# Optimization experiments

Measured on AMD Instinct MI355X. Metric: run time of the kernel, lower is better.

## Reference

```python
import jax, jax.numpy as jnp
import numpy as np
import math

_DENSE_LOCAL_W = 64
_DYADIC = [96, 128, 192, 256, 384, 512, 768, 1024, 1536]
OFFSETS = sorted(set(range(0, _DENSE_LOCAL_W + 1)) | set(_DYADIC))  # 74 offsets

B, N, D, H = 1, 2048, 1024, 16
HD = D // H


def setup_inputs() -> dict:
    key = jax.random.key(0)
    ks = jax.random.split(key, 8)
    s = 1.0 / math.sqrt(D)
    x = jax.random.normal(ks[0], (B, N, D), dtype=jnp.float32)
    Wqkv = jax.random.uniform(ks[1], (3 * D, D), jnp.float32, -s, s)
    bqkv = jax.random.uniform(ks[2], (3 * D,), jnp.float32, -s, s)
    Wgate = jax.random.uniform(ks[3], (D, D), jnp.float32, -s, s)
    bgate = jax.random.uniform(ks[4], (D,), jnp.float32, -s, s)
    Wout = jax.random.uniform(ks[5], (D, D), jnp.float32, -s, s)
    bout = jax.random.uniform(ks[6], (D,), jnp.float32, -s, s)
    # pos_bias init exactly as in the module: -log(1+delta) * alpha_h, shape (O, H)
    alphas = jnp.linspace(0.2, 2.0, H)
    deltas = jnp.array([math.log(1.0 + d) for d in OFFSETS], dtype=jnp.float32)
    pos_bias = -deltas[:, None] * alphas[None, :]
    offsets = jnp.array(OFFSETS, dtype=jnp.int32)
    return {"x": x, "Wqkv": Wqkv, "bqkv": bqkv, "Wgate": Wgate, "bgate": bgate,
            "Wout": Wout, "bout": bout, "pos_bias": pos_bias, "offsets": offsets}


def reference(x, Wqkv, bqkv, Wgate, bgate, Wout, bout, pos_bias, offsets):
    Bx, Nx, Dx = x.shape
    qkv = x @ Wqkv.T + bqkv                       # (B, N, 3D)
    q, k, v = jnp.split(qkv, 3, axis=-1)
    q = q.reshape(Bx, Nx, H, HD).transpose(0, 2, 1, 3)  # (B, H, N, HD)
    k = k.reshape(Bx, Nx, H, HD).transpose(0, 2, 1, 3)
    v = v.reshape(Bx, Nx, H, HD).transpose(0, 2, 1, 3)
    scale = HD ** -0.5

    # gather shifted K/V: position n attends to n - delta for each fixed offset
    n_idx = jnp.arange(Nx, dtype=jnp.int32)[:, None]      # (N, 1)
    idx = n_idx - offsets[None, :]                        # (N, O)
    valid = idx >= 0                                      # (N, O)
    idx_c = jnp.clip(idx, 0, Nx - 1)
    K_all = k[:, :, idx_c, :]                             # (B, H, N, O, HD)
    V_all = v[:, :, idx_c, :]

    scores = jnp.einsum('bhnd,bhnod->bhno', q, K_all) * scale
    scores = scores + pos_bias.T[None, :, None, :]        # (1, H, 1, O)
    scores = jnp.where(valid[None, None], scores, -jnp.inf)
    alpha = jax.nn.softmax(scores, axis=-1)               # (B, H, N, O)
    out = jnp.einsum('bhno,bhnod->bhnd', alpha, V_all)    # (B, H, N, HD)

    flat = out.transpose(0, 2, 1, 3).reshape(Bx, Nx, Dx)  # (B, N, D)
    gate = jax.nn.sigmoid(x @ Wgate.T + bgate)
    return (flat * gate) @ Wout.T + bout                  # dropout = identity (eval)
```

## Files before the change

### kernel.cpp

```cpp
#include <hip/hip_runtime.h>
#include <hip/hip_bf16.h>

#define SEQ_N 2048
#define DIM   1024
#define NHEAD 16
#define HDIM  64
#define LDQ   4096
#define NOFF  74
#define NDENSE 65
#define NJ    224
#define NT    16
#define PST   232
#define QST   88

typedef __attribute__((ext_vector_type(8))) __bf16 bv8;
typedef __attribute__((ext_vector_type(4))) __bf16 bv4;
typedef __attribute__((ext_vector_type(4))) float  f32x4;

typedef __attribute__((address_space(3))) void as3_void;
typedef __attribute__((address_space(1))) void as1_void;

__device__ __forceinline__ void async16(const void* g, void* l) {
  __builtin_amdgcn_global_load_lds((as1_void*)(unsigned long long)g,
                                   (as3_void*)l, 16, 0, 0);
}

#define E1 (SEQ_N * DIM)
#define E2 (E1 + 3 * DIM * DIM)
#define E3 (E2 + DIM * DIM)
#define E4 (E3 + DIM * DIM)
__global__ __launch_bounds__(256) void cvt_all(
    const float* __restrict__ x, const float* __restrict__ wqkv,
    const float* __restrict__ wgate, const float* __restrict__ wout,
    __bf16* __restrict__ dst) {
  long i = ((long)blockIdx.x * 256 + threadIdx.x) * 4;
  if (i >= E4) return;
  const float* s; long o;
  if (i < E1)      { s = x;     o = i; }
  else if (i < E2) { s = wqkv;  o = i - E1; }
  else if (i < E3) { s = wgate; o = i - E2; }
  else             { s = wout;  o = i - E3; }
  float4 v = *(const float4*)(s + o);
  bv4 ov;
  ov[0] = (__bf16)v.x; ov[1] = (__bf16)v.y; ov[2] = (__bf16)v.z; ov[3] = (__bf16)v.w;
  *(bv4*)(dst + i) = ov;
}

#define BM 128
#define BK 32

template <int BN_, typename OutT>
__global__ __launch_bounds__(256) void gemm_bt(
    const __bf16* __restrict__ A, const __bf16* __restrict__ B1,
    const __bf16* __restrict__ B2, const float* __restrict__ bias1,
    const float* __restrict__ bias2, int Nsplit,
    OutT* __restrict__ C, int ldc, int K) {
  __shared__ __attribute__((aligned(16))) __bf16 Asm[BM * BK];
  __shared__ __attribute__((aligned(16))) __bf16 Bsm[BN_ * BK];
  constexpr int NJT = BN_ / 32;
  constexpr int CA = BM * BK / 8;
  constexpr int CB = BN_ * BK / 8;

  const int tid  = threadIdx.x;
  const int lane = tid & 63;
  const int wave = tid >> 6;
  const int wr = wave >> 1, wc = wave & 1;
  const int fr = lane & 15, fq = lane >> 4;

  const int bn0 = blockIdx.x * BN_;
  const int bm0 = blockIdx.y * BM;

  const __bf16* Bp;
  const float* biasp;
  if (bn0 < Nsplit) { Bp = B1 + (size_t)bn0 * K;            biasp = bias1 + bn0; }
  else              { Bp = B2 + (size_t)(bn0 - Nsplit) * K; biasp = bias2 + (bn0 - Nsplit); }
  const __bf16* Ap = A + (size_t)bm0 * K;

  f32x4 acc[4][NJT] = {};

  for (int kt = 0; kt < K; kt += BK) {
    __syncthreads();
#pragma unroll
    for (int c0 = 0; c0 < CA + CB; c0 += 256) {
      int c = c0 + tid;
      if (c < CA) {
        int rr = c >> 2, qq = c & 3;
        async16(Ap + (size_t)rr * K + kt + qq * 8, Asm + c * 8);
      } else {
        int cb = c - CA;
        int rr = cb >> 2, qq = cb & 3;
        async16(Bp + (size_t)rr * K + kt + qq * 8, Bsm + cb * 8);
      }
    }
    __syncthreads();

    bv8 af[4], bfr[NJT];
#pragma unroll
    for (int i = 0; i < 4; ++i)
      af[i] = *(const bv8*)(Asm + (wr * 64 + i * 16 + fr) * BK + fq * 8);
#pragma unroll
    for (int j = 0; j < NJT; ++j)
      bfr[j] = *(const bv8*)(Bsm + (wc * (BN_ / 2) + j * 16 + fr) * BK + fq * 8);
#pragma unroll
    for (int i = 0; i < 4; ++i)
#pragma unroll
      for (int j = 0; j < NJT; ++j)
        acc[i][j] = __builtin_amdgcn_mfma_f32_16x16x32_bf16(af[i], bfr[j], acc[i][j], 0, 0, 0);
  }

#pragma unroll
  for (int i = 0; i < 4; ++i) {
#pragma unroll
    for (int j = 0; j < NJT; ++j) {
      int ccol = wc * (BN_ / 2) + j * 16 + fr;
      float b = biasp[ccol];
#pragma unroll
      for (int r = 0; r < 4; ++r) {
        int row = bm0 + wr * 64 + i * 16 + fq * 4 + r;
        C[(size_t)row * ldc + bn0 + ccol] = (OutT)(acc[i][j][r] + b);
      }
    }
  }
}

__global__ __launch_bounds__(256) void attn_mfma(
    const __bf16* __restrict__ qkv,
    const float* __restrict__ pos_bias,
    const int* __restrict__ offsets,
    __bf16* __restrict__ fg) {
  const int n0 = (blockIdx.x >> 4) * NT;
  const int h  = blockIdx.x & 15;
  const int tid = threadIdx.x;
  const int lane = tid & 63;
  const int w = tid >> 6;
  const int fr = lane & 15, fq = lane >> 4;

  __shared__ __attribute__((aligned(16))) __bf16 Kbuf[NJ * HDIM];
  __shared__ __attribute__((aligned(16))) __bf16 Vbuf[NJ * HDIM];
  __shared__ __attribute__((aligned(16))) __bf16 Qbuf[NT * QST];
  __shared__ __attribute__((aligned(16))) float  Sbuf[NT][80];
  __shared__ __attribute__((aligned(16))) __bf16 Pd[NT * PST];
  __shared__ float inv_l[NT];

  if (tid < 128) {
    int ni = tid >> 3, ch = tid & 7;
    bv8 q = *(const bv8*)(qkv + (size_t)(n0 + ni) * LDQ + h * HDIM + ch * 8);
    *(bv8*)(Qbuf + ni * QST + ch * 8) = q;
  }
#pragma unroll
  for (int c0 = 0; c0 < NT * PST / 8; c0 += 256) {
    int c = c0 + tid;
    if (c < NT * PST / 8) *(uint4*)(Pd + c * 8) = make_uint4(0, 0, 0, 0);
  }
  {
    int ch = lane & 7;
#pragma unroll
    for (int it = 0; it < 7; ++it) {
      int jbase = it * 32 + w * 8;
      int j = jbase + (lane >> 3);
      int g;
      if (j < 80) g = n0 - 64 + j;
      else { int jj = j - 80; g = n0 - offsets[NDENSE + (jj >> 4)] + (jj & 15); }
      if (g < 0) g = 0;
      const __bf16* kg = qkv + (size_t)g * LDQ + DIM + h * HDIM + ch * 8;
      async16(kg, Kbuf + jbase * HDIM + lane * 8);
      async16(kg + DIM, Vbuf + jbase * HDIM + lane * 8);
    }
  }
  __syncthreads();

  for (int jb = w; jb < 14; jb += 4) {
    f32x4 acc = {};
#pragma unroll
    for (int kk = 0; kk < 2; ++kk) {
      bv8 a = *(const bv8*)(Qbuf + fr * QST + kk * 32 + fq * 8);
      bv8 b = *(const bv8*)(Kbuf + (jb * 16 + fr) * HDIM + kk * 32 + fq * 8);
      acc = __builtin_amdgcn_mfma_f32_16x16x32_bf16(a, b, acc, 0, 0, 0);
    }
    int j = jb * 16 + fr;
    if (jb < 5) {
      bool gvalid = (n0 - 64 + j) >= 0;
#pragma unroll
      for (int r = 0; r < 4; ++r) {
        int ni = fq * 4 + r;
        int o = ni + 64 - j;
        if (o >= 0 && o < NDENSE)
          Sbuf[ni][o] = gvalid ? acc[r] : -3.0e38f;
      }
    } else {
      int jj = j - 80;
      int s = jj >> 4, tni = jj & 15;
      int r = tni - fq * 4;
      if (r >= 0 && r < 4) {
        bool gvalid = (n0 + tni - offsets[NDENSE + s]) >= 0;
        Sbuf[tni][NDENSE + s] = gvalid ? acc[r] : -3.0e38f;
      }
    }
  }
  __syncthreads();

  {
    int t = tid & 15, ni = tid >> 4;
    float sc5[5];
    float m = -3.0e38f;
#pragma unroll
    for (int k = 0; k < 5; ++k) {
      int o = t + k * 16;
      float v = -3.0e38f;
      if (o < NOFF) {
        float raw = Sbuf[ni][o];
        if (raw > -1.0e38f) v = raw * 0.125f + pos_bias[o * NHEAD + h];
      }
      sc5[k] = v;
      m = fmaxf(m, v);
    }
#pragma unroll
    for (int d = 1; d < 16; d <<= 1) m = fmaxf(m, __shfl_xor(m, d));
    float sum = 0.f;
#pragma unroll
    for (int k = 0; k < 5; ++k) {
      int o = t + k * 16;
      if (o < NOFF && sc5[k] > -1.0e38f) {
        float e = __expf(sc5[k] - m);
        sum += e;
        int j = (o < NDENSE) ? (ni + 64 - o) : (80 + (o - NDENSE) * 16 + ni);
        Pd[ni * PST + j] = (__bf16)e;
      }
    }
#pragma unroll
    for (int d = 1; d < 16; d <<= 1) sum += __shfl_xor(sum, d);
    if (t == 0) inv_l[ni] = 1.f / sum;
  }
  __syncthreads();

  {
    const int db = w;
    f32x4 acc = {};
#pragma unroll
    for (int kt = 0; kt < 7; ++kt) {
      bv8 a = *(const bv8*)(Pd + fr * PST + kt * 32 + fq * 8);
      bv8 b;
#pragma unroll
      for (int jj = 0; jj < 8; ++jj)
        b[jj] = Vbuf[(kt * 32 + fq * 8 + jj) * HDIM + db * 16 + fr];
      acc = __builtin_amdgcn_mfma_f32_16x16x32_bf16(a, b, acc, 0, 0, 0);
    }
    int d = db * 16 + fr;
#pragma unroll
    for (int r = 0; r < 4; ++r) {
      int ni = fq * 4 + r;
      float o = acc[r] * inv_l[ni];
      float gp = (float)qkv[(size_t)(n0 + ni) * LDQ + 3 * DIM + h * HDIM + d];
      float gate = 1.f / (1.f + __expf(-gp));
      fg[(size_t)(n0 + ni) * DIM + h * HDIM + d] = (__bf16)(o * gate);
    }
  }
}

extern "C" void kernel_launch(void* const* d_in, const int* in_sizes, int n_in,
                              void* d_out, int out_size, void* d_ws, size_t ws_size,
                              hipStream_t stream) {
  const float* x        = (const float*)d_in[0];
  const float* Wqkv     = (const float*)d_in[1];
  const float* bqkv     = (const float*)d_in[2];
  const float* Wgate    = (const float*)d_in[3];
  const float* bgate    = (const float*)d_in[4];
  const float* Wout     = (const float*)d_in[5];
  const float* bout     = (const float*)d_in[6];
  const float* pos_bias = (const float*)d_in[7];
  const int*   offsets  = (const int*)d_in[8];
  float* out = (float*)d_out;

  __bf16* xb       = (__bf16*)d_ws;
  __bf16* Wqkvb    = xb    + (size_t)SEQ_N * DIM;
  __bf16* Wgateb   = Wqkvb + (size_t)3 * DIM * DIM;
  __bf16* Woutb    = Wgateb + (size_t)DIM * DIM;
  __bf16* qkvg     = Woutb + (size_t)DIM * DIM;
  __bf16* flatgate = qkvg + (size_t)SEQ_N * LDQ;

  cvt_all<<<dim3(E4 / 1024), dim3(256), 0, stream>>>(x, Wqkv, Wgate, Wout, xb);

  gemm_bt<128, __bf16><<<dim3(LDQ / 128, SEQ_N / BM), dim3(256), 0, stream>>>(
      xb, Wqkvb, Wgateb, bqkv, bgate, 3 * DIM, qkvg, LDQ, DIM);

  attn_mfma<<<dim3((SEQ_N / NT) * NHEAD), dim3(256), 0, stream>>>(
      qkvg, pos_bias, offsets, flatgate);

  gemm_bt<64, float><<<dim3(DIM / 64, SEQ_N / BM), dim3(256), 0, stream>>>(
      flatgate, Woutb, Woutb, bout, bout, 1 << 30, out, DIM, DIM);
}
```

Baseline: 161.2 us.

## Store V transposed in LDS and remap GEMM tiles across XCDs

The attention kernel now loads V through registers and writes it transposed into shared memory. This lets the PV MFMA read its B operand with one 16-byte vector load instead of eight scalar strided LDS reads. The cost is synchronous global loads, replacing the async direct-to-LDS path for V, plus extra packing ALU work. Separately, the GEMM block index is remapped so consecutive blocks on each XCD cover contiguous column chunks, which is meant to improve L2 reuse of the B operand.

```diff
diff --git a/kernel.cpp b/kernel.cpp
--- a/kernel.cpp
+++ b/kernel.cpp
@@ -11,6 +11,7 @@
 #define NJ    224
 #define NT    16
 #define PST   232
+#define TST   232
 #define QST   88
 
 typedef __attribute__((ext_vector_type(8))) __bf16 bv8;
@@ -67,8 +68,11 @@
   const int wr = wave >> 1, wc = wave & 1;
   const int fr = lane & 15, fq = lane >> 4;
 
-  const int bn0 = blockIdx.x * BN_;
-  const int bm0 = blockIdx.y * BM;
+  int flat = blockIdx.y * gridDim.x + blockIdx.x;
+  int nch  = gridDim.x >> 3;
+  int xcd  = flat & 7, loc = flat >> 3;
+  const int bn0 = (xcd * nch + (loc % nch)) * BN_;
+  const int bm0 = (loc / nch) * BM;
 
   const __bf16* Bp;
   const float* biasp;
@@ -136,7 +140,7 @@
   const int fr = lane & 15, fq = lane >> 4;
 
   __shared__ __attribute__((aligned(16))) __bf16 Kbuf[NJ * HDIM];
-  __shared__ __attribute__((aligned(16))) __bf16 Vbuf[NJ * HDIM];
+  __shared__ __attribute__((aligned(16))) __bf16 VbufT[HDIM * TST];
   __shared__ __attribute__((aligned(16))) __bf16 Qbuf[NT * QST];
   __shared__ __attribute__((aligned(16))) float  Sbuf[NT][80];
   __shared__ __attribute__((aligned(16))) __bf16 Pd[NT * PST];
@@ -162,9 +166,33 @@
       if (j < 80) g = n0 - 64 + j;
       else { int jj = j - 80; g = n0 - offsets[NDENSE + (jj >> 4)] + (jj & 15); }
       if (g < 0) g = 0;
-      const __bf16* kg = qkv + (size_t)g * LDQ + DIM + h * HDIM + ch * 8;
-      async16(kg, Kbuf + jbase * HDIM + lane * 8);
-      async16(kg + DIM, Vbuf + jbase * HDIM + lane * 8);
+      async16(qkv + (size_t)g * LDQ + DIM + h * HDIM + ch * 8,
+              Kbuf + jbase * HDIM + lane * 8);
+    }
+  }
+  {
+    int a = tid >> 5, p = tid & 31;
+#pragma unroll
+    for (int it = 0; it < 4; ++it) {
+      int pj = it * 32 + p;
+      if (pj < NJ / 2) {
+        int j0 = pj * 2;
+        int g0;
+        if (j0 < 80) g0 = n0 - 64 + j0;
+        else { int jj = j0 - 80; g0 = n0 - offsets[NDENSE + (jj >> 4)] + (jj & 15); }
+        int g1 = g0 + 1;
+        if (g0 < 0) g0 = 0;
+        if (g1 < 0) g1 = 0;
+        bv8 v0 = *(const bv8*)(qkv + (size_t)g0 * LDQ + 2 * DIM + h * HDIM + a * 8);
+        bv8 v1 = *(const bv8*)(qkv + (size_t)g1 * LDQ + 2 * DIM + h * HDIM + a * 8);
+        const unsigned short* u0 = (const unsigned short*)&v0;
+        const unsigned short* u1 = (const unsigned short*)&v1;
+#pragma unroll
+        for (int i = 0; i < 8; ++i) {
+          unsigned pk = (unsigned)u0[i] | ((unsigned)u1[i] << 16);
+          *(unsigned*)(VbufT + (a * 8 + i) * TST + j0) = pk;
+        }
+      }
     }
   }
   __syncthreads();
@@ -239,10 +267,7 @@
 #pragma unroll
     for (int kt = 0; kt < 7; ++kt) {
       bv8 a = *(const bv8*)(Pd + fr * PST + kt * 32 + fq * 8);
-      bv8 b;
-#pragma unroll
-      for (int jj = 0; jj < 8; ++jj)
-        b[jj] = Vbuf[(kt * 32 + fq * 8 + jj) * HDIM + db * 16 + fr];
+      bv8 b = *(const bv8*)(VbufT + (db * 16 + fr) * TST + kt * 32 + fq * 8);
       acc = __builtin_amdgcn_mfma_f32_16x16x32_bf16(a, b, acc, 0, 0, 0);
     }
     int d = db * 16 + fr;
```

Result: slower. 168.0 us (+4.2%).
